# Performance work log

Hardware: AMD Instinct MI355X
Metric: run time of the kernel (lower is better)

## Reference

```python
import jax, jax.numpy as jnp
import numpy as np

N = 4096        # nodes
E = 131072      # edges (avg degree 32)
IN = 512        # in_channels
HID = 512       # hidden_channels
HEADS = 4       # GAT heads
LAYERS = 3      # residual GCN layers
G = 16          # graphs in batch
OUT = 1         # out_channels
NEG_SLOPE = 0.2 # GAT LeakyReLU slope


def setup_inputs() -> dict:
    key = jax.random.key(0)
    ks = jax.random.split(key, 9)
    s = 0.02
    x = jax.random.normal(ks[0], (N, IN), dtype=jnp.float32)
    edge_index = jax.random.randint(ks[1], (2, E), 0, N)
    batch = jnp.sort(jax.random.randint(ks[2], (N,), 0, G))
    W_gat = jax.random.normal(ks[3], (HEADS, IN, HID), dtype=jnp.float32) * s
    a_src = jax.random.normal(ks[4], (HEADS, HID), dtype=jnp.float32) * s
    a_dst = jax.random.normal(ks[5], (HEADS, HID), dtype=jnp.float32) * s
    W_gcn = jax.random.normal(ks[6], (LAYERS, HID, HID), dtype=jnp.float32) * s
    fc_w = jax.random.normal(ks[7], (HID, OUT), dtype=jnp.float32) * s
    fc_b = jnp.zeros((OUT,), dtype=jnp.float32)
    return {"x": x, "edge_index": edge_index, "batch": batch,
            "W_gat": W_gat, "a_src": a_src, "a_dst": a_dst,
            "W_gcn": W_gcn, "fc_w": fc_w, "fc_b": fc_b}


def reference(x, edge_index, batch, W_gat, a_src, a_dst, W_gcn, fc_w, fc_b):
    src, dst = edge_index[0], edge_index[1]

    # ---- LatentRelationCapturerGAT: multi-head GAT, one output per head ----
    h = jnp.einsum('nc,hcd->nhd', x, W_gat)                    # [N,H,D]
    lg_src = jnp.einsum('nhd,hd->nh', h, a_src)                # [N,H]
    lg_dst = jnp.einsum('nhd,hd->nh', h, a_dst)                # [N,H]
    e = jax.nn.leaky_relu(lg_src[src] + lg_dst[dst], NEG_SLOPE)  # [E,H]
    # segment softmax over incoming edges of each destination node
    m = jax.ops.segment_max(e, dst, num_segments=N)            # [N,H]
    w = jnp.exp(e - m[dst])                                    # [E,H]
    z = jax.ops.segment_sum(w, dst, num_segments=N)            # [N,H]
    alpha = w / (z[dst] + 1e-16)                               # [E,H]
    H0 = jax.ops.segment_sum(alpha[:, :, None] * h[src], dst, num_segments=N)  # [N,H,D]

    # ---- dense adjacency build + GCN normalization (shared across heads) ----
    A = jnp.zeros((N, N), dtype=x.dtype).at[src, dst].set(1.0)
    A = A + jnp.eye(N, dtype=x.dtype)                          # self-loops
    dinv = jax.lax.rsqrt(jnp.sum(A, axis=1))                   # deg >= 1
    A_hat = dinv[:, None] * A * dinv[None, :]                  # D^-1/2 (A+I) D^-1/2

    # ---- DeepResidualGCN: H <- relu(A_hat @ H @ W_l) + H (heads batched) ----
    H = H0
    for l in range(W_gcn.shape[0]):
        P = jnp.einsum('nm,mhd->nhd', A_hat, H)                # propagate
        H = jax.nn.relu(jnp.einsum('nhd,de->nhe', P, W_gcn[l])) + H

    # ---- per-head global mean pool, then mean over heads ----
    ones = jnp.ones((N,), dtype=x.dtype)
    cnt = jnp.maximum(jax.ops.segment_sum(ones, batch, num_segments=G), 1.0)  # [G]
    pooled = jax.ops.segment_sum(H, batch, num_segments=G) / cnt[:, None, None]  # [G,H,D]
    feats = pooled.mean(axis=1)                                # [G,D]

    return feats @ fc_w + fc_b                                 # [G,OUT]
```

## Files before the change

### kernel.cpp

```cpp
#include <hip/hip_runtime.h>
#include <cstdint>
#include <cstddef>

#define Nn    4096
#define Ee    131072
#define INC   512
#define HIDC  512
#define HEADS 4
#define NLAY  3
#define GG    16
#define FW    2048

typedef __attribute__((ext_vector_type(8))) short bfrag;
typedef __attribute__((ext_vector_type(4))) float ffrag;

__device__ __forceinline__ ushort f2bf(float v){
  uint u = __builtin_bit_cast(uint, v);
  u += 0x7fffu + ((u>>16)&1u);
  return (ushort)(u>>16);
}
__device__ __forceinline__ float bf2f(ushort s){
  uint u = ((uint)s)<<16; return __builtin_bit_cast(float, u);
}
__device__ __forceinline__ void fma8(float* acc, uint4 g, float w){
  uint u[4] = {g.x, g.y, g.z, g.w};
  #pragma unroll
  for (int q=0;q<4;q++){
    float lo = __builtin_bit_cast(float, u[q]<<16);
    float hi = __builtin_bit_cast(float, u[q] & 0xffff0000u);
    acc[2*q]   += w*lo;
    acc[2*q+1] += w*hi;
  }
}
__device__ __forceinline__ void pack8(void* p, const float* a){
  uint4 o;
  o.x = (uint)f2bf(a[0]) | ((uint)f2bf(a[1])<<16);
  o.y = (uint)f2bf(a[2]) | ((uint)f2bf(a[3])<<16);
  o.z = (uint)f2bf(a[4]) | ((uint)f2bf(a[5])<<16);
  o.w = (uint)f2bf(a[6]) | ((uint)f2bf(a[7])<<16);
  *(uint4*)p = o;
}

__global__ __launch_bounds__(256) void tobf(const float* __restrict__ X, ushort* __restrict__ Xb){
  int i = blockIdx.x*256 + threadIdx.x;
  Xb[i] = f2bf(X[i]);
}

__global__ __launch_bounds__(256) void tbf(const float* __restrict__ W, ushort* __restrict__ T){
  __shared__ float tile[32][33];
  int b = blockIdx.z;
  int r0 = blockIdx.y*32, c0 = blockIdx.x*32;
  int t = threadIdx.x;
  int i = t>>3, j0 = (t&7)*4;
  const float* Wb = W + (size_t)b*512*512;
  float4 v = *(const float4*)(Wb + (size_t)(r0+i)*512 + c0 + j0);
  tile[i][j0]=v.x; tile[i][j0+1]=v.y; tile[i][j0+2]=v.z; tile[i][j0+3]=v.w;
  __syncthreads();
  ushort* o = T + (size_t)b*512*512 + (size_t)(c0+i)*512 + r0 + j0;
  #pragma unroll
  for (int q=0;q<4;q++) o[q] = f2bf(tile[j0+q][i]);
}

__global__ __launch_bounds__(256) void gemm_bf(
    const ushort* __restrict__ A, const ushort* __restrict__ B,
    const float* __restrict__ Res, float* __restrict__ Cf, ushort* __restrict__ Cb,
    int M, int N, int K, int relu_res)
{
  __shared__ __align__(16) ushort Ah[2][2048];
  __shared__ __align__(16) ushort Bh[2][4096];
  int t = threadIdx.x;
  int m0 = blockIdx.y*64, n0 = blockIdx.x*128;
  int srA = t>>2, kqA = t&3;
  const ushort* pA = A + (size_t)(m0+srA)*K + kqA*8;
  int wA = (kqA*64 + srA)*8;
  int srB = t>>1, cB = t&1;
  const ushort* pB = B + (size_t)(n0+srB)*K + cB*16;
  int wB0 = ((2*cB)*128 + srB)*8;
  int wB1 = wB0 + 1024;

  int wave = t>>6, lane = t&63;
  int wm = (wave&1)*32, wn = (wave>>1)*64;
  int lm = lane&15, quad = lane>>4;

  ffrag acc[2][4];
  #pragma unroll
  for (int i=0;i<2;i++){
    #pragma unroll
    for (int j=0;j<4;j++) acc[i][j] = (ffrag){0.f,0.f,0.f,0.f};
  }

  uint4 ra  = *(const uint4*)(pA);
  uint4 rb0 = *(const uint4*)(pB);  uint4 rb1 = *(const uint4*)(pB+8);
  *(uint4*)&Ah[0][wA]  = ra;
  *(uint4*)&Bh[0][wB0] = rb0; *(uint4*)&Bh[0][wB1] = rb1;
  if (K > 32){
    ra  = *(const uint4*)(pA+32);
    rb0 = *(const uint4*)(pB+32); rb1 = *(const uint4*)(pB+40);
  }
  __syncthreads();

  for (int k0 = 0; k0 < K; k0 += 32){
    int cur = (k0>>5)&1, nxt = cur^1;
    bfrag af[2];
    #pragma unroll
    for (int mt=0; mt<2; mt++)
      af[mt] = *(const bfrag*)&Ah[cur][(quad*64 + wm + mt*16 + lm)*8];
    #pragma unroll
    for (int nt=0; nt<4; nt++){
      bfrag bf = *(const bfrag*)&Bh[cur][(quad*128 + wn + nt*16 + lm)*8];
      #pragma unroll
      for (int mt=0; mt<2; mt++)
        acc[mt][nt] = __builtin_amdgcn_mfma_f32_16x16x32_bf16(af[mt], bf, acc[mt][nt], 0,0,0);
    }
    if (k0+32 < K){
      *(uint4*)&Ah[nxt][wA]  = ra;
      *(uint4*)&Bh[nxt][wB0] = rb0; *(uint4*)&Bh[nxt][wB1] = rb1;
      if (k0+64 < K){
        ra  = *(const uint4*)(pA+k0+64);
        rb0 = *(const uint4*)(pB+k0+64); rb1 = *(const uint4*)(pB+k0+72);
      }
    }
    __syncthreads();
  }

  #pragma unroll
  for (int mt=0; mt<2; mt++){
    #pragma unroll
    for (int nt=0; nt<4; nt++){
      #pragma unroll
      for (int r=0;r<4;r++){
        int grow = m0 + wm + mt*16 + quad*4 + r;
        int gcol = n0 + wn + nt*16 + lm;
        size_t off = (size_t)grow*N + gcol;
        float v = acc[mt][nt][r];
        if (relu_res) v = fmaxf(v,0.f) + Res[off];
        if (Cf) Cf[off] = v;
        if (Cb) Cb[off] = f2bf(v);
      }
    }
  }
}

__global__ __launch_bounds__(256) void compute_lg(const ushort* __restrict__ hbf,
    const float* __restrict__ a_src, const float* __restrict__ a_dst,
    float* __restrict__ lgs, float* __restrict__ lgd){
  int n = blockIdx.x; int t = threadIdx.x;
  int hd = t>>6, lane = t&63;
  uint4 g = *(const uint4*)(hbf + (size_t)n*FW + hd*HIDC + lane*8);
  float h[8] = {0,0,0,0,0,0,0,0};
  fma8(h, g, 1.0f);
  float4 as0 = *(const float4*)(a_src + hd*HIDC + lane*8);
  float4 as1 = *(const float4*)(a_src + hd*HIDC + lane*8 + 4);
  float4 ad0 = *(const float4*)(a_dst + hd*HIDC + lane*8);
  float4 ad1 = *(const float4*)(a_dst + hd*HIDC + lane*8 + 4);
  float s1 = h[0]*as0.x + h[1]*as0.y + h[2]*as0.z + h[3]*as0.w
           + h[4]*as1.x + h[5]*as1.y + h[6]*as1.z + h[7]*as1.w;
  float s2 = h[0]*ad0.x + h[1]*ad0.y + h[2]*ad0.z + h[3]*ad0.w
           + h[4]*ad1.x + h[5]*ad1.y + h[6]*ad1.z + h[7]*ad1.w;
  for (int off=32; off; off>>=1){ s1 += __shfl_down(s1,off); s2 += __shfl_down(s2,off); }
  if (lane==0){ lgs[n*HEADS+hd]=s1; lgd[n*HEADS+hd]=s2; }
}

__global__ __launch_bounds__(256) void edge_pass1(const int* __restrict__ src, const int* __restrict__ dst,
    int* __restrict__ indeg, unsigned int* __restrict__ bitmap,
    int* __restrict__ cnt_s, int* __restrict__ flag){
  int e = blockIdx.x*256+threadIdx.x; if (e>=Ee) return;
  int s = src[e], d = dst[e];
  atomicAdd(&indeg[d],1);
  unsigned int key = (unsigned int)s*Nn + (unsigned int)d;
  unsigned int bit = 1u<<(key&31);
  unsigned int old = atomicOr(&bitmap[key>>5], bit);
  int f = (old & bit) ? 0 : 1;
  flag[e] = f;
  if (f) atomicAdd(&cnt_s[s],1);
}

__global__ __launch_bounds__(1024) void exscan2(const int* __restrict__ cnt0, int* __restrict__ rp0,
    const int* __restrict__ cnt1, int* __restrict__ rp1){
  const int* cnt = blockIdx.x ? cnt1 : cnt0;
  int* rowptr    = blockIdx.x ? rp1  : rp0;
  __shared__ int sums[1024];
  int t = threadIdx.x;
  int v[4]; int s=0;
  #pragma unroll
  for (int i=0;i<4;i++){ int idx=t*4+i; v[i] = cnt[idx]; s+=v[i]; }
  sums[t]=s; __syncthreads();
  for (int off=1; off<1024; off<<=1){
    int other = (t>=off)? sums[t-off] : 0;
    __syncthreads();
    sums[t] += other;
    __syncthreads();
  }
  int run = (t>0)? sums[t-1] : 0;
  #pragma unroll
  for (int i=0;i<4;i++){ int idx=t*4+i; rowptr[idx]=run; run+=v[i]; }
  if (t==1023) rowptr[Nn]=sums[1023];
}

__global__ __launch_bounds__(256) void compute_dinv(const int* __restrict__ cnt, float* __restrict__ dinv){
  int n = blockIdx.x*256+threadIdx.x; if (n<Nn) dinv[n] = 1.0f/sqrtf((float)(1+cnt[n]));
}

__global__ __launch_bounds__(256) void edge_pass2(const int* __restrict__ src, const int* __restrict__ dst,
    const int* __restrict__ flag,
    const int* __restrict__ rp_d, int* __restrict__ fill_d, int* __restrict__ slist,
    const int* __restrict__ rp_s, int* __restrict__ fill_s, int2* __restrict__ cw,
    const float* __restrict__ dinv){
  int e = blockIdx.x*256+threadIdx.x; if (e>=Ee) return;
  int s = src[e], d = dst[e];
  int p = atomicAdd(&fill_d[d],1); slist[rp_d[d]+p] = s;
  if (flag[e]){
    int q = atomicAdd(&fill_s[s],1);
    cw[rp_s[s]+q] = make_int2(d, __float_as_int(dinv[d]));
  }
}

__global__ __launch_bounds__(256) void gat_aggregate(const ushort* __restrict__ hbf,
    const float* __restrict__ lgs, const float* __restrict__ lgd,
    const int* __restrict__ rowptr, const int* __restrict__ slist,
    float* __restrict__ Hfeat, ushort* __restrict__ Hbf){
  int t = threadIdx.x;
  int wv = __builtin_amdgcn_readfirstlane(t>>6);
  int lane = t&63;
  int b = blockIdx.x;
  int hd = __builtin_amdgcn_readfirstlane(b & 3);
  int n = ((b>>2)<<2) + wv;
  int beg = rowptr[n], deg = rowptr[n+1]-beg;
  float ldst = lgd[n*HEADS+hd];
  float m_ = -3.4e38f, z_ = 0.f;
  int   s0 = 0; float v0 = 0.f;
  for (int i=lane; i<deg; i+=64){
    int s = slist[beg+i];
    float v = lgs[s*HEADS+hd] + ldst;
    v = v>0.f ? v : 0.2f*v;
    if (i<64){ s0=s; v0=v; }
    float mn = fmaxf(m_, v);
    z_ = z_*__expf(m_-mn) + __expf(v-mn);
    m_ = mn;
  }
  for (int o=32;o;o>>=1){
    float mo = __shfl_down(m_,o), zo = __shfl_down(z_,o);
    float mn = fmaxf(m_, mo);
    z_ = z_*__expf(m_-mn) + zo*__expf(mo-mn);
    m_ = mn;
  }
  float mx = __shfl(m_,0);
  float zs = __shfl(z_,0);
  float inv = 1.f/(zs+1e-16f);
  float acc[8] = {0,0,0,0,0,0,0,0};
  const ushort* hb = hbf + hd*HIDC + lane*8;
  for (int base=0; base<deg; base+=64){
    float al; int s;
    if (base==0){
      s = s0;
      al = (lane<deg) ? __expf(v0-mx)*inv : 0.f;
    } else {
      int i = base+lane;
      al = 0.f; s = 0;
      if (i<deg){
        s = slist[beg+i];
        float v = lgs[s*HEADS+hd] + ldst; v = v>0.f ? v : 0.2f*v;
        al = __expf(v-mx)*inv;
      }
    }
    int cn = min(64, deg-base);
    int c = 0;
    for (; c+8<=cn; c+=8){
      uint4 g[8]; float a[8];
      #pragma unroll
      for (int q=0;q<8;q++){
        a[q] = __shfl(al,c+q);
        int ss = __shfl(s,c+q);
        g[q] = *(const uint4*)(hb + (size_t)ss*FW);
      }
      #pragma unroll
      for (int q=0;q<8;q++) fma8(acc, g[q], a[q]);
    }
    for (; c+4<=cn; c+=4){
      uint4 g[4]; float a[4];
      #pragma unroll
      for (int q=0;q<4;q++){
        a[q] = __shfl(al,c+q);
        int ss = __shfl(s,c+q);
        g[q] = *(const uint4*)(hb + (size_t)ss*FW);
      }
      #pragma unroll
      for (int q=0;q<4;q++) fma8(acc, g[q], a[q]);
    }
    for (; c<cn; c++){
      float a = __shfl(al,c);
      int ss  = __shfl(s,c);
      uint4 g = *(const uint4*)(hb + (size_t)ss*FW);
      fma8(acc, g, a);
    }
  }
  size_t off = (size_t)n*FW + hd*HIDC + lane*8;
  *(float4*)(Hfeat + off)     = make_float4(acc[0],acc[1],acc[2],acc[3]);
  *(float4*)(Hfeat + off + 4) = make_float4(acc[4],acc[5],acc[6],acc[7]);
  pack8(Hbf + off, acc);
}

__global__ __launch_bounds__(256) void spmm_bf(const ushort* __restrict__ Hbf,
    ushort* __restrict__ Phi,
    const int* __restrict__ rowptr, const int2* __restrict__ cw, const float* __restrict__ dinv){
  int t = threadIdx.x;
  int wv = __builtin_amdgcn_readfirstlane(t>>6);
  int lane = t&63;
  int b = blockIdx.x;
  int ck = __builtin_amdgcn_readfirstlane(b & 3);
  int n = ((b>>2)<<2) + wv;
  int f = (ck<<9) + lane*8;
  float di = dinv[n];
  float acc[8] = {0,0,0,0,0,0,0,0};
  const ushort* hb = Hbf + f;
  uint4 self = *(const uint4*)(hb + (size_t)n*FW);
  fma8(acc, self, di*di);
  int beg = rowptr[n], end = rowptr[n+1];
  for (int base=beg; base<end; base+=64){
    int i = base + lane;
    int m = n; float w = 0.f;
    if (i < end){ int2 e = cw[i]; m = e.x; w = di*__int_as_float(e.y); }
    int cn = min(64, end-base);
    int c = 0;
    for (; c+8<=cn; c+=8){
      uint4 g[8]; float ww[8];
      #pragma unroll
      for (int q=0;q<8;q++){
        ww[q] = __shfl(w,c+q);
        int mm = __shfl(m,c+q);
        g[q] = *(const uint4*)(hb + (size_t)mm*FW);
      }
      #pragma unroll
      for (int q=0;q<8;q++) fma8(acc, g[q], ww[q]);
    }
    for (; c+4<=cn; c+=4){
      uint4 g[4]; float ww[4];
      #pragma unroll
      for (int q=0;q<4;q++){
        ww[q] = __shfl(w,c+q);
        int mm = __shfl(m,c+q);
        g[q] = *(const uint4*)(hb + (size_t)mm*FW);
      }
      #pragma unroll
      for (int q=0;q<4;q++) fma8(acc, g[q], ww[q]);
    }
    for (; c<cn; c++){
      int mm   = __shfl(m,c);
      float ww = __shfl(w,c);
      uint4 g = *(const uint4*)(hb + (size_t)mm*FW);
      fma8(acc, g, ww);
    }
  }
  pack8(Phi + (size_t)n*FW + f, acc);
}

__global__ __launch_bounds__(256) void graph_offsets(const int* __restrict__ batch, int* __restrict__ goff){
  __shared__ int cnt[GG];
  int t = threadIdx.x;
  if (t<GG) cnt[t]=0;
  __syncthreads();
  for (int i=t;i<Nn;i+=256) atomicAdd(&cnt[batch[i]],1);
  __syncthreads();
  if (t==0){ int run=0; for (int g=0; g<GG; g++){ goff[g]=run; run+=cnt[g]; } goff[GG]=run; }
}
__global__ __launch_bounds__(256) void pool_accum(const float* __restrict__ H,
    const int* __restrict__ batch, float* __restrict__ psum){
  int d = blockIdx.y*256 + threadIdx.x;
  int n0 = blockIdx.x*32;
  int g = batch[n0];
  float s = 0.f;
  for (int k=0;k<32;k++){
    int n = n0+k;
    int gn = batch[n];
    if (gn != g){ atomicAdd(&psum[(size_t)g*FW+d], s); s=0.f; g=gn; }
    s += H[(size_t)n*FW + d];
  }
  atomicAdd(&psum[(size_t)g*FW+d], s);
}
__global__ __launch_bounds__(256) void final_out(const float* __restrict__ psum,
    const int* __restrict__ goff,
    const float* __restrict__ fc_w, const float* __restrict__ fc_b, float* __restrict__ out){
  int g = blockIdx.x; int t = threadIdx.x;
  float cinv = 0.25f / fmaxf((float)(goff[g+1]-goff[g]), 1.f);
  float p = 0.f;
  for (int d=t; d<HIDC; d+=256){
    float f = cinv*(psum[(size_t)g*FW+d] + psum[(size_t)g*FW+HIDC+d]
                  + psum[(size_t)g*FW+2*HIDC+d] + psum[(size_t)g*FW+3*HIDC+d]);
    p += f*fc_w[d];
  }
  __shared__ float red[4];
  for (int off=32; off; off>>=1) p += __shfl_down(p,off);
  if ((t&63)==0) red[t>>6]=p;
  __syncthreads();
  if (t==0) out[g] = red[0]+red[1]+red[2]+red[3] + fc_b[0];
}

extern "C" void kernel_launch(void* const* d_in, const int* in_sizes, int n_in,
                              void* d_out, int out_size, void* d_ws, size_t ws_size,
                              hipStream_t stream){
  const float* x      = (const float*)d_in[0];
  const int*   ei     = (const int*)d_in[1];
  const int*   batch  = (const int*)d_in[2];
  const float* W_gat  = (const float*)d_in[3];
  const float* a_src  = (const float*)d_in[4];
  const float* a_dst  = (const float*)d_in[5];
  const float* W_gcn  = (const float*)d_in[6];
  const float* fc_w   = (const float*)d_in[7];
  const float* fc_b   = (const float*)d_in[8];
  float* out = (float*)d_out;
  const int* src = ei;
  const int* dst = ei + Ee;

  char* w = (char*)d_ws;
  size_t off = 0;
  auto alloc = [&](size_t bytes)->char*{ char* p = w + off; off = (off + bytes + 255) & ~(size_t)255; return p; };
  float*  Hfeat  = (float*)alloc((size_t)Nn*FW*4);
  ushort* hbf    = (ushort*)alloc((size_t)Nn*FW*2);
  ushort* Hbf    = (ushort*)alloc((size_t)Nn*FW*2);
  ushort* Xbf    = (ushort*)alloc((size_t)Nn*INC*2);
  ushort* WgatT  = (ushort*)alloc((size_t)HEADS*INC*HIDC*2);
  ushort* WgcnT  = (ushort*)alloc((size_t)NLAY*HIDC*HIDC*2);
  float* lgs    = (float*)alloc((size_t)Nn*HEADS*4);
  float* lgd    = (float*)alloc((size_t)Nn*HEADS*4);
  int* indeg    = (int*)alloc(Nn*4);
  int* fill_d   = (int*)alloc(Nn*4);
  int* cnt_s    = (int*)alloc(Nn*4);
  int* fill_s   = (int*)alloc(Nn*4);
  float* psum   = (float*)alloc((size_t)GG*FW*4);
  unsigned int* bitmap = (unsigned int*)alloc((size_t)Nn*Nn/8);
  size_t zero_bytes = (size_t)Nn*4*4 + (size_t)GG*FW*4 + (size_t)Nn*Nn/8;
  int* rowptr_d = (int*)alloc((Nn+1)*4);
  int* slist    = (int*)alloc(Ee*4);
  int* rowptr_s = (int*)alloc((Nn+1)*4);
  int2* cwlist  = (int2*)alloc((size_t)Ee*8);
  int* flag     = (int*)alloc(Ee*4);
  float* dinv   = (float*)alloc(Nn*4);
  int* goff     = (int*)alloc((GG+1)*4);
  ushort* Phi   = hbf;

  hipMemsetAsync(indeg, 0, zero_bytes, stream);

  tobf<<<(Nn*INC)/256,256,0,stream>>>(x, Xbf);
  tbf<<<dim3(16,16,HEADS),256,0,stream>>>(W_gat, WgatT);
  tbf<<<dim3(16,16,NLAY),256,0,stream>>>(W_gcn, WgcnT);

  gemm_bf<<<dim3(FW/128, Nn/64),256,0,stream>>>(Xbf, WgatT,
      nullptr, nullptr, hbf, Nn, FW, INC, 0);
  compute_lg<<<Nn,256,0,stream>>>(hbf, a_src, a_dst, lgs, lgd);

  edge_pass1<<<Ee/256,256,0,stream>>>(src, dst, indeg, bitmap, cnt_s, flag);
  exscan2<<<2,1024,0,stream>>>(indeg, rowptr_d, cnt_s, rowptr_s);
  compute_dinv<<<Nn/256,256,0,stream>>>(cnt_s, dinv);
  edge_pass2<<<Ee/256,256,0,stream>>>(src, dst, flag, rowptr_d, fill_d, slist,
                                      rowptr_s, fill_s, cwlist, dinv);
  gat_aggregate<<<Nn,256,0,stream>>>(hbf, lgs, lgd, rowptr_d, slist, Hfeat, Hbf);

  for (int l=0;l<NLAY;l++){
    spmm_bf<<<Nn,256,0,stream>>>(Hbf, Phi, rowptr_s, cwlist, dinv);
    gemm_bf<<<dim3(HIDC/128, (Nn*HEADS)/64),256,0,stream>>>(Phi,
        WgcnT + (size_t)l*HIDC*HIDC,
        Hfeat, Hfeat, (l==NLAY-1)? nullptr : Hbf, Nn*HEADS, HIDC, HIDC, 1);
  }

  graph_offsets<<<1,256,0,stream>>>(batch, goff);
  pool_accum<<<dim3(Nn/32, FW/256),256,0,stream>>>(Hfeat, batch, psum);
  final_out<<<GG,256,0,stream>>>(psum, goff, fc_w, fc_b, out);
}
```

Before: 396.2 us.

## Drop fp32 residual feature buffer and keep hidden state only in bf16

Removes the fp32 Hfeat copy of the node features. The GAT output, the residual adds in each GCN layer and the pooling input now all use the bf16 Hbf buffer. This cuts global memory traffic from fp32 writes and reads in gat_aggregate, the three GEMM epilogues and pool_accum. In exchange the residual stream accumulates in bf16, which adds rounding error across layers, and the GEMM now reads and writes the same buffer in place.

After: 379.6 us. -4.2%, faster.

```diff
diff --git a/kernel.cpp b/kernel.cpp
--- a/kernel.cpp
+++ b/kernel.cpp
@@ -63,7 +63,7 @@
 
 __global__ __launch_bounds__(256) void gemm_bf(
     const ushort* __restrict__ A, const ushort* __restrict__ B,
-    const float* __restrict__ Res, float* __restrict__ Cf, ushort* __restrict__ Cb,
+    const ushort* Res, ushort* Cb,
     int M, int N, int K, int relu_res)
 {
   __shared__ __align__(16) ushort Ah[2][2048];
@@ -133,9 +133,8 @@
         int gcol = n0 + wn + nt*16 + lm;
         size_t off = (size_t)grow*N + gcol;
         float v = acc[mt][nt][r];
-        if (relu_res) v = fmaxf(v,0.f) + Res[off];
-        if (Cf) Cf[off] = v;
-        if (Cb) Cb[off] = f2bf(v);
+        if (relu_res) v = fmaxf(v,0.f) + bf2f(Res[off]);
+        Cb[off] = f2bf(v);
       }
     }
   }
@@ -218,7 +217,7 @@
 __global__ __launch_bounds__(256) void gat_aggregate(const ushort* __restrict__ hbf,
     const float* __restrict__ lgs, const float* __restrict__ lgd,
     const int* __restrict__ rowptr, const int* __restrict__ slist,
-    float* __restrict__ Hfeat, ushort* __restrict__ Hbf){
+    ushort* __restrict__ Hbf){
   int t = threadIdx.x;
   int wv = __builtin_amdgcn_readfirstlane(t>>6);
   int lane = t&63;
@@ -295,8 +294,6 @@
     }
   }
   size_t off = (size_t)n*FW + hd*HIDC + lane*8;
-  *(float4*)(Hfeat + off)     = make_float4(acc[0],acc[1],acc[2],acc[3]);
-  *(float4*)(Hfeat + off + 4) = make_float4(acc[4],acc[5],acc[6],acc[7]);
   pack8(Hbf + off, acc);
 }
 
@@ -363,19 +360,26 @@
   __syncthreads();
   if (t==0){ int run=0; for (int g=0; g<GG; g++){ goff[g]=run; run+=cnt[g]; } goff[GG]=run; }
 }
-__global__ __launch_bounds__(256) void pool_accum(const float* __restrict__ H,
+__global__ __launch_bounds__(256) void pool_accum(const ushort* __restrict__ Hb,
     const int* __restrict__ batch, float* __restrict__ psum){
-  int d = blockIdx.y*256 + threadIdx.x;
+  int d2 = blockIdx.y*256 + threadIdx.x;
   int n0 = blockIdx.x*32;
   int g = batch[n0];
-  float s = 0.f;
+  float s0 = 0.f, s1 = 0.f;
   for (int k=0;k<32;k++){
     int n = n0+k;
     int gn = batch[n];
-    if (gn != g){ atomicAdd(&psum[(size_t)g*FW+d], s); s=0.f; g=gn; }
-    s += H[(size_t)n*FW + d];
-  }
-  atomicAdd(&psum[(size_t)g*FW+d], s);
+    if (gn != g){
+      atomicAdd(&psum[(size_t)g*FW + d2*2],   s0);
+      atomicAdd(&psum[(size_t)g*FW + d2*2+1], s1);
+      s0=0.f; s1=0.f; g=gn;
+    }
+    uint v = *(const uint*)(Hb + (size_t)n*FW + d2*2);
+    s0 += bf2f((ushort)(v&0xffff));
+    s1 += bf2f((ushort)(v>>16));
+  }
+  atomicAdd(&psum[(size_t)g*FW + d2*2],   s0);
+  atomicAdd(&psum[(size_t)g*FW + d2*2+1], s1);
 }
 __global__ __launch_bounds__(256) void final_out(const float* __restrict__ psum,
     const int* __restrict__ goff,
@@ -414,7 +418,6 @@
   char* w = (char*)d_ws;
   size_t off = 0;
   auto alloc = [&](size_t bytes)->char*{ char* p = w + off; off = (off + bytes + 255) & ~(size_t)255; return p; };
-  float*  Hfeat  = (float*)alloc((size_t)Nn*FW*4);
   ushort* hbf    = (ushort*)alloc((size_t)Nn*FW*2);
   ushort* Hbf    = (ushort*)alloc((size_t)Nn*FW*2);
   ushort* Xbf    = (ushort*)alloc((size_t)Nn*INC*2);
@@ -445,7 +448,7 @@
   tbf<<<dim3(16,16,NLAY),256,0,stream>>>(W_gcn, WgcnT);
 
   gemm_bf<<<dim3(FW/128, Nn/64),256,0,stream>>>(Xbf, WgatT,
-      nullptr, nullptr, hbf, Nn, FW, INC, 0);
+      nullptr, hbf, Nn, FW, INC, 0);
   compute_lg<<<Nn,256,0,stream>>>(hbf, a_src, a_dst, lgs, lgd);
 
   edge_pass1<<<Ee/256,256,0,stream>>>(src, dst, indeg, bitmap, cnt_s, flag);
@@ -453,16 +456,16 @@
   compute_dinv<<<Nn/256,256,0,stream>>>(cnt_s, dinv);
   edge_pass2<<<Ee/256,256,0,stream>>>(src, dst, flag, rowptr_d, fill_d, slist,
                                       rowptr_s, fill_s, cwlist, dinv);
-  gat_aggregate<<<Nn,256,0,stream>>>(hbf, lgs, lgd, rowptr_d, slist, Hfeat, Hbf);
+  gat_aggregate<<<Nn,256,0,stream>>>(hbf, lgs, lgd, rowptr_d, slist, Hbf);
 
   for (int l=0;l<NLAY;l++){
     spmm_bf<<<Nn,256,0,stream>>>(Hbf, Phi, rowptr_s, cwlist, dinv);
     gemm_bf<<<dim3(HIDC/128, (Nn*HEADS)/64),256,0,stream>>>(Phi,
         WgcnT + (size_t)l*HIDC*HIDC,
-        Hfeat, Hfeat, (l==NLAY-1)? nullptr : Hbf, Nn*HEADS, HIDC, HIDC, 1);
+        Hbf, Hbf, Nn*HEADS, HIDC, HIDC, 1);
   }
 
   graph_offsets<<<1,256,0,stream>>>(batch, goff);
-  pool_accum<<<dim3(Nn/32, FW/256),256,0,stream>>>(Hfeat, batch, psum);
+  pool_accum<<<dim3(Nn/32, FW/512),256,0,stream>>>(Hbf, batch, psum);
   final_out<<<GG,256,0,stream>>>(psum, goff, fc_w, fc_b, out);
 }
```
